# Kernel optimization log

Hardware: AMD Instinct MI355X
Metric: run time of the kernel (lower is better)

## Reference

```python
import jax, jax.numpy as jnp
import numpy as np

B, S, D_IN, D_OUT = 4, 2048, 2048, 2048
EPS = 1e-10


def setup_inputs() -> dict:
    key = jax.random.key(0)
    kx, kw, kb = jax.random.split(key, 3)
    x = jax.random.normal(kx, (B, S, D_IN), dtype=jnp.float32)
    weight = jax.random.normal(kw, (D_OUT, D_IN), dtype=jnp.float32) * 0.02
    bias = jax.random.normal(kb, (D_OUT,), dtype=jnp.float32) * 0.02
    return {"x": x, "weight": weight, "bias": bias}


def reference(x, weight, bias):
    # abs-mean scale over the whole weight matrix (scalar)
    scale = jnp.mean(jnp.abs(weight))
    # ternary quantization: round(w/scale) clamped to {-1, 0, 1}
    w_t = jnp.clip(jnp.round(weight / (scale + EPS)), -1.0, 1.0)
    # straight-through estimator: forward uses w_t*scale, grad flows to weight
    w_ste = weight + jax.lax.stop_gradient(w_t * scale - weight)
    # F.linear: x @ w_ste.T + bias
    return jnp.einsum('bsi,oi->bso', x, w_ste) + bias
```

## Files before the change

kernel.cpp:

```cpp
#include <hip/hip_runtime.h>
#include <hip/hip_bf16.h>
#include <stdint.h>

#define M_DIM 8192
#define N_DIM 2048
#define K_DIM 2048
#define NT    (K_DIM / 64)

typedef float f32x4 __attribute__((ext_vector_type(4)));
typedef short bf16x8 __attribute__((ext_vector_type(8)));

typedef const __attribute__((address_space(1))) char* gp_t;
typedef __attribute__((address_space(3))) char* lp_t;

static __device__ __forceinline__ void gload_lds16(const void* g, void* l) {
  __builtin_amdgcn_global_load_lds((gp_t)(uintptr_t)g, (lp_t)(uint32_t)(uintptr_t)l, 16, 0, 0);
}

static __device__ __forceinline__ unsigned short f2bf(float f) {
  unsigned int u = __float_as_uint(f);
  unsigned int r = (u + 0x7FFFu + ((u >> 16) & 1u)) >> 16;
  return (unsigned short)r;
}

__global__ void absum_partials(const float* __restrict__ w, float* __restrict__ partials) {
  int tid = blockIdx.x * 256 + threadIdx.x;
  const float4* w4 = (const float4*)w;
  float s = 0.f;
#pragma unroll
  for (int i = 0; i < 4; ++i) {
    float4 v = w4[tid + i * 262144];
    s += fabsf(v.x) + fabsf(v.y) + fabsf(v.z) + fabsf(v.w);
  }
#pragma unroll
  for (int off = 32; off > 0; off >>= 1) s += __shfl_down(s, off, 64);
  __shared__ float ls[4];
  if ((threadIdx.x & 63) == 0) ls[threadIdx.x >> 6] = s;
  __syncthreads();
  if (threadIdx.x == 0) partials[blockIdx.x] = (ls[0] + ls[1]) + (ls[2] + ls[3]);
}

__global__ void finalize_scale(const float* __restrict__ partials, float* __restrict__ scale_out) {
  float s = 0.f;
#pragma unroll
  for (int i = 0; i < 4; ++i) s += partials[threadIdx.x + i * 256];
#pragma unroll
  for (int off = 32; off > 0; off >>= 1) s += __shfl_down(s, off, 64);
  __shared__ float ls[4];
  if ((threadIdx.x & 63) == 0) ls[threadIdx.x >> 6] = s;
  __syncthreads();
  if (threadIdx.x == 0)
    scale_out[0] = ((ls[0] + ls[1]) + (ls[2] + ls[3])) * (1.0f / 4194304.0f);
}

__global__ void quant_w(const float* __restrict__ w, const float* __restrict__ scale_p,
                        unsigned short* __restrict__ wt) {
  const float inv = 1.0f / (scale_p[0] + 1e-10f);
  int tid = blockIdx.x * 256 + threadIdx.x;
  float4 v = ((const float4*)w)[tid];
  ushort4 o;
  float t;
  t = fminf(1.f, fmaxf(-1.f, rintf(v.x * inv))); o.x = f2bf(t);
  t = fminf(1.f, fmaxf(-1.f, rintf(v.y * inv))); o.y = f2bf(t);
  t = fminf(1.f, fmaxf(-1.f, rintf(v.z * inv))); o.z = f2bf(t);
  t = fminf(1.f, fmaxf(-1.f, rintf(v.w * inv))); o.w = f2bf(t);
  ((ushort4*)wt)[tid] = o;
}

__global__ void cvt_x(const float* __restrict__ x, unsigned short* __restrict__ xb) {
  int tid = blockIdx.x * 256 + threadIdx.x;
  float4 v = ((const float4*)x)[tid];
  ushort4 o;
  o.x = f2bf(v.x); o.y = f2bf(v.y); o.z = f2bf(v.z); o.w = f2bf(v.w);
  ((ushort4*)xb)[tid] = o;
}


#define VMCNT(n) asm volatile("s_waitcnt vmcnt(" #n ")" ::: "memory")
#define FENCE    asm volatile("" ::: "memory")
#define BARRIER  do { FENCE; __builtin_amdgcn_s_barrier(); FENCE; } while (0)

#define READ_A(mh)                                                                          \
  do {                                                                                      \
    _Pragma("unroll") for (int i = 0; i < 4; ++i) {                                         \
      a_r[i][0] = *(const bf16x8*)(curA + (wr * 128 + (mh) * 64 + i * 16) * 128 + rd_off);  \
      a_r[i][1] = *(const bf16x8*)(curA + (wr * 128 + (mh) * 64 + i * 16) * 128 + 64 + rd_off); \
    }                                                                                       \
  } while (0)

#define READ_B(nh, br)                                                                      \
  do {                                                                                      \
    _Pragma("unroll") for (int j = 0; j < 2; ++j) {                                         \
      br[j][0] = *(const bf16x8*)(curB + (wc * 64 + (nh) * 32 + j * 16) * 128 + rd_off);    \
      br[j][1] = *(const bf16x8*)(curB + (wc * 64 + (nh) * 32 + j * 16) * 128 + 64 + rd_off); \
    }                                                                                       \
  } while (0)

#define MFMA_PH(mh, nh, br)                                                                 \
  do {                                                                                      \
    __builtin_amdgcn_s_setprio(1);                                                          \
    _Pragma("unroll") for (int i = 0; i < 4; ++i)                                           \
      _Pragma("unroll") for (int j = 0; j < 2; ++j)                                         \
        acc[(mh) * 4 + i][(nh) * 2 + j] = __builtin_amdgcn_mfma_f32_16x16x32_bf16(          \
            a_r[i][0], br[j][0], acc[(mh) * 4 + i][(nh) * 2 + j], 0, 0, 0);                 \
    _Pragma("unroll") for (int i = 0; i < 4; ++i)                                           \
      _Pragma("unroll") for (int j = 0; j < 2; ++j)                                         \
        acc[(mh) * 4 + i][(nh) * 2 + j] = __builtin_amdgcn_mfma_f32_16x16x32_bf16(          \
            a_r[i][1], br[j][1], acc[(mh) * 4 + i][(nh) * 2 + j], 0, 0, 0);                 \
    __builtin_amdgcn_s_setprio(0);                                                          \
  } while (0)

#define SA(bufsel, r) gload_lds16(Ag + offA[r] + ktA, ldsb + (bufsel) * 65536 + tid * 16 + (r) * 8192)
#define SB(bufsel, r) gload_lds16(Bg + offB[r] + ktB, ldsb + (bufsel) * 65536 + 32768 + tid * 16 + (r) * 8192)

__global__ void __launch_bounds__(512, 2)
gemm_bt(const unsigned short* __restrict__ A, const unsigned short* __restrict__ Bt,
        const float* __restrict__ bias, const float* __restrict__ scale_p,
        float* __restrict__ out) {
  __shared__ __align__(16) char lds_raw[131072];
  char* ldsb = (char*)lds_raw;

  const int tid = threadIdx.x;
  const int lane = tid & 63;
  const int wid = tid >> 6;
  const int wr = wid >> 2;
  const int wc = wid & 3;
  const int l15 = lane & 15, lhi = lane >> 4;
  const int rd_off = l15 * 128 + ((lhi * 16) ^ (((l15 >> 2) & 1) << 5));

  const int bid = blockIdx.x;
  const int swz = (bid & 7) * 32 + (bid >> 3);
  const int bm = swz >> 3;
  const int bn = swz & 7;
  const int m0 = bm << 8, n0 = bn << 8;

  const int srow = tid >> 3;
  const int scol = ((tid & 7) << 4) ^ (((tid >> 5) & 1) << 5);
  const char* Ag = (const char*)A;
  const char* Bg = (const char*)Bt;
  uint32_t offA[4], offB[4];
#pragma unroll
  for (int r = 0; r < 4; ++r) {
    offA[r] = (uint32_t)(m0 + srow + r * 64) * (K_DIM * 2) + scol;
    offB[r] = (uint32_t)(n0 + srow + r * 64) * (K_DIM * 2) + scol;
  }
  uint32_t ktA = 0, ktB = 0;

  f32x4 acc[8][4];
#pragma unroll
  for (int m = 0; m < 8; ++m)
#pragma unroll
    for (int n = 0; n < 4; ++n) {
      f32x4 z = {0.f, 0.f, 0.f, 0.f};
      acc[m][n] = z;
    }

  SA(0, 0); SA(0, 1); SA(0, 2); SA(0, 3);
  SB(0, 0); SB(0, 1); SB(0, 2); SB(0, 3);
  ktB = 128;
  SB(1, 0); SB(1, 1); SB(1, 2); SB(1, 3);
  ktA = 128; ktB = 256;
  VMCNT(4);
  BARRIER;

  bf16x8 a_r[4][2], b0[2][2], b1[2][2];

  for (int t = 0; t < NT; ++t) {
    const int cb = t & 1;
    const char* curA = ldsb + cb * 65536;
    const char* curB = curA + 32768;

    READ_A(0);
    READ_B(0, b0);
    if (t < NT - 1) { SA(cb ^ 1, 0); SA(cb ^ 1, 1); }
    BARRIER;
    MFMA_PH(0, 0, b0);
    BARRIER;

    READ_B(1, b1);
    if (t < NT - 1) { SA(cb ^ 1, 2); SA(cb ^ 1, 3); ktA += 128; }
    BARRIER;
    MFMA_PH(0, 1, b1);
    BARRIER;

    READ_A(1);
    if (t < NT - 2) { SB(cb, 0); SB(cb, 1); }
    BARRIER;
    MFMA_PH(1, 0, b0);
    BARRIER;

    if (t < NT - 2) {
      SB(cb, 2); SB(cb, 3); ktB += 128;
      VMCNT(4);
    } else {
      VMCNT(0);
    }
    BARRIER;
    MFMA_PH(1, 1, b1);
    BARRIER;
  }

  const float scale = scale_p[0];
#pragma unroll
  for (int n = 0; n < 4; ++n) {
    const int col = n0 + wc * 64 + n * 16 + l15;
    const float bv = bias[col];
#pragma unroll
    for (int m = 0; m < 8; ++m) {
      const int r0 = m0 + wr * 128 + m * 16 + lhi * 4;
      float* op = out + (size_t)r0 * N_DIM + col;
#pragma unroll
      for (int j = 0; j < 4; ++j) op[(size_t)j * N_DIM] = acc[m][n][j] * scale + bv;
    }
  }
}

extern "C" void kernel_launch(void* const* d_in, const int* in_sizes, int n_in,
                              void* d_out, int out_size, void* d_ws, size_t ws_size,
                              hipStream_t stream) {
  (void)in_sizes; (void)n_in; (void)out_size; (void)ws_size;
  const float* x    = (const float*)d_in[0];
  const float* w    = (const float*)d_in[1];
  const float* bias = (const float*)d_in[2];
  float* out = (float*)d_out;

  float* partials = (float*)d_ws;
  float* scale_slot = partials + 1024;
  unsigned short* wt = (unsigned short*)((char*)d_ws + 8192);
  unsigned short* xb = (unsigned short*)((char*)d_ws + 8192 + (size_t)N_DIM * K_DIM * 2);

  absum_partials<<<1024, 256, 0, stream>>>(w, partials);
  finalize_scale<<<1, 256, 0, stream>>>(partials, scale_slot);
  quant_w<<<4096, 256, 0, stream>>>(w, scale_slot, wt);
  cvt_x<<<16384, 256, 0, stream>>>(x, xb);
  gemm_bt<<<256, 512, 0, stream>>>(xb, wt, bias, scale_slot, out);
}
```

Baseline: 100.4 us.

## Fuse preprocessing kernels and switch LDS swizzle to full XOR pattern

Merges the x-to-bf16 conversion and the weight abs-sum partials into one launch, and folds the scale finalization into every quant_w block so each block re-reduces the 1024 partials itself. This cuts the preprocessing from four launches to two, removing launch gaps and the serial single-block finalize step. It also changes the GEMM's LDS store and read swizzle from a single-bit XOR to a 3-bit row XOR to reduce bank conflicts on ds_read. The cost is redundant partial reductions in each quant block.

```diff
diff --git a/kernel.cpp b/kernel.cpp
--- a/kernel.cpp
+++ b/kernel.cpp
@@ -23,39 +23,47 @@
   return (unsigned short)r;
 }
 
-__global__ void absum_partials(const float* __restrict__ w, float* __restrict__ partials) {
-  int tid = blockIdx.x * 256 + threadIdx.x;
-  const float4* w4 = (const float4*)w;
+__global__ void cvt_x_absum(const float* __restrict__ x, unsigned short* __restrict__ xb,
+                            const float* __restrict__ w, float* __restrict__ partials) {
+  const int b = blockIdx.x;
+  if (b < 16384) {
+    int tid = b * 256 + threadIdx.x;
+    float4 v = ((const float4*)x)[tid];
+    ushort4 o;
+    o.x = f2bf(v.x); o.y = f2bf(v.y); o.z = f2bf(v.z); o.w = f2bf(v.w);
+    ((ushort4*)xb)[tid] = o;
+  } else {
+    int tid = (b - 16384) * 256 + threadIdx.x;
+    const float4* w4 = (const float4*)w;
+    float s = 0.f;
+#pragma unroll
+    for (int i = 0; i < 4; ++i) {
+      float4 v = w4[tid + i * 262144];
+      s += fabsf(v.x) + fabsf(v.y) + fabsf(v.z) + fabsf(v.w);
+    }
+#pragma unroll
+    for (int off = 32; off > 0; off >>= 1) s += __shfl_down(s, off, 64);
+    __shared__ float ls[4];
+    if ((threadIdx.x & 63) == 0) ls[threadIdx.x >> 6] = s;
+    __syncthreads();
+    if (threadIdx.x == 0) partials[b - 16384] = (ls[0] + ls[1]) + (ls[2] + ls[3]);
+  }
+}
+
+__global__ void quant_w(const float* __restrict__ w, const float* __restrict__ partials,
+                        unsigned short* __restrict__ wt, float* __restrict__ scale_out) {
+  __shared__ float ls[4];
   float s = 0.f;
 #pragma unroll
-  for (int i = 0; i < 4; ++i) {
-    float4 v = w4[tid + i * 262144];
-    s += fabsf(v.x) + fabsf(v.y) + fabsf(v.z) + fabsf(v.w);
-  }
+  for (int i = 0; i < 4; ++i) s += partials[threadIdx.x + i * 256];
 #pragma unroll
   for (int off = 32; off > 0; off >>= 1) s += __shfl_down(s, off, 64);
-  __shared__ float ls[4];
   if ((threadIdx.x & 63) == 0) ls[threadIdx.x >> 6] = s;
   __syncthreads();
-  if (threadIdx.x == 0) partials[blockIdx.x] = (ls[0] + ls[1]) + (ls[2] + ls[3]);
-}
-
-__global__ void finalize_scale(const float* __restrict__ partials, float* __restrict__ scale_out) {
-  float s = 0.f;
-#pragma unroll
-  for (int i = 0; i < 4; ++i) s += partials[threadIdx.x + i * 256];
-#pragma unroll
-  for (int off = 32; off > 0; off >>= 1) s += __shfl_down(s, off, 64);
-  __shared__ float ls[4];
-  if ((threadIdx.x & 63) == 0) ls[threadIdx.x >> 6] = s;
-  __syncthreads();
-  if (threadIdx.x == 0)
-    scale_out[0] = ((ls[0] + ls[1]) + (ls[2] + ls[3])) * (1.0f / 4194304.0f);
-}
-
-__global__ void quant_w(const float* __restrict__ w, const float* __restrict__ scale_p,
-                        unsigned short* __restrict__ wt) {
-  const float inv = 1.0f / (scale_p[0] + 1e-10f);
+  const float scale = ((ls[0] + ls[1]) + (ls[2] + ls[3])) * (1.0f / 4194304.0f);
+  if (blockIdx.x == 0 && threadIdx.x == 0) scale_out[0] = scale;
+
+  const float inv = 1.0f / (scale + 1e-10f);
   int tid = blockIdx.x * 256 + threadIdx.x;
   float4 v = ((const float4*)w)[tid];
   ushort4 o;
@@ -67,47 +75,39 @@
   ((ushort4*)wt)[tid] = o;
 }
 
-__global__ void cvt_x(const float* __restrict__ x, unsigned short* __restrict__ xb) {
-  int tid = blockIdx.x * 256 + threadIdx.x;
-  float4 v = ((const float4*)x)[tid];
-  ushort4 o;
-  o.x = f2bf(v.x); o.y = f2bf(v.y); o.z = f2bf(v.z); o.w = f2bf(v.w);
-  ((ushort4*)xb)[tid] = o;
-}
-
 
 #define VMCNT(n) asm volatile("s_waitcnt vmcnt(" #n ")" ::: "memory")
 #define FENCE    asm volatile("" ::: "memory")
 #define BARRIER  do { FENCE; __builtin_amdgcn_s_barrier(); FENCE; } while (0)
 
-#define READ_A(mh)                                                                          \
-  do {                                                                                      \
-    _Pragma("unroll") for (int i = 0; i < 4; ++i) {                                         \
-      a_r[i][0] = *(const bf16x8*)(curA + (wr * 128 + (mh) * 64 + i * 16) * 128 + rd_off);  \
-      a_r[i][1] = *(const bf16x8*)(curA + (wr * 128 + (mh) * 64 + i * 16) * 128 + 64 + rd_off); \
-    }                                                                                       \
+#define READ_A(mh)                                                                              \
+  do {                                                                                          \
+    _Pragma("unroll") for (int i = 0; i < 4; ++i) {                                             \
+      a_r[i][0] = *(const bf16x8*)(curA + (wr * 128 + (mh) * 64 + i * 16) * 128 + rd0);         \
+      a_r[i][1] = *(const bf16x8*)(curA + (wr * 128 + (mh) * 64 + i * 16) * 128 + rd1);         \
+    }                                                                                           \
   } while (0)
 
-#define READ_B(nh, br)                                                                      \
-  do {                                                                                      \
-    _Pragma("unroll") for (int j = 0; j < 2; ++j) {                                         \
-      br[j][0] = *(const bf16x8*)(curB + (wc * 64 + (nh) * 32 + j * 16) * 128 + rd_off);    \
-      br[j][1] = *(const bf16x8*)(curB + (wc * 64 + (nh) * 32 + j * 16) * 128 + 64 + rd_off); \
-    }                                                                                       \
+#define READ_B(nh, br)                                                                          \
+  do {                                                                                          \
+    _Pragma("unroll") for (int j = 0; j < 2; ++j) {                                             \
+      br[j][0] = *(const bf16x8*)(curB + (wc * 64 + (nh) * 32 + j * 16) * 128 + rd0);           \
+      br[j][1] = *(const bf16x8*)(curB + (wc * 64 + (nh) * 32 + j * 16) * 128 + rd1);           \
+    }                                                                                           \
   } while (0)
 
-#define MFMA_PH(mh, nh, br)                                                                 \
-  do {                                                                                      \
-    __builtin_amdgcn_s_setprio(1);                                                          \
-    _Pragma("unroll") for (int i = 0; i < 4; ++i)                                           \
-      _Pragma("unroll") for (int j = 0; j < 2; ++j)                                         \
-        acc[(mh) * 4 + i][(nh) * 2 + j] = __builtin_amdgcn_mfma_f32_16x16x32_bf16(          \
-            a_r[i][0], br[j][0], acc[(mh) * 4 + i][(nh) * 2 + j], 0, 0, 0);                 \
-    _Pragma("unroll") for (int i = 0; i < 4; ++i)                                           \
-      _Pragma("unroll") for (int j = 0; j < 2; ++j)                                         \
-        acc[(mh) * 4 + i][(nh) * 2 + j] = __builtin_amdgcn_mfma_f32_16x16x32_bf16(          \
-            a_r[i][1], br[j][1], acc[(mh) * 4 + i][(nh) * 2 + j], 0, 0, 0);                 \
-    __builtin_amdgcn_s_setprio(0);                                                          \
+#define MFMA_PH(mh, nh, br)                                                                     \
+  do {                                                                                          \
+    __builtin_amdgcn_s_setprio(1);                                                              \
+    _Pragma("unroll") for (int i = 0; i < 4; ++i)                                               \
+      _Pragma("unroll") for (int j = 0; j < 2; ++j)                                             \
+        acc[(mh) * 4 + i][(nh) * 2 + j] = __builtin_amdgcn_mfma_f32_16x16x32_bf16(              \
+            a_r[i][0], br[j][0], acc[(mh) * 4 + i][(nh) * 2 + j], 0, 0, 0);                     \
+    _Pragma("unroll") for (int i = 0; i < 4; ++i)                                               \
+      _Pragma("unroll") for (int j = 0; j < 2; ++j)                                             \
+        acc[(mh) * 4 + i][(nh) * 2 + j] = __builtin_amdgcn_mfma_f32_16x16x32_bf16(              \
+            a_r[i][1], br[j][1], acc[(mh) * 4 + i][(nh) * 2 + j], 0, 0, 0);                     \
+    __builtin_amdgcn_s_setprio(0);                                                              \
   } while (0)
 
 #define SA(bufsel, r) gload_lds16(Ag + offA[r] + ktA, ldsb + (bufsel) * 65536 + tid * 16 + (r) * 8192)
@@ -126,7 +126,10 @@
   const int wr = wid >> 2;
   const int wc = wid & 3;
   const int l15 = lane & 15, lhi = lane >> 4;
-  const int rd_off = l15 * 128 + ((lhi * 16) ^ (((l15 >> 2) & 1) << 5));
+
+  const int swzl = (l15 & 7) << 4;
+  const int rd0 = l15 * 128 + ((lhi * 16) ^ swzl);
+  const int rd1 = l15 * 128 + (((lhi * 16) ^ 64) ^ swzl);
 
   const int bid = blockIdx.x;
   const int swz = (bid & 7) * 32 + (bid >> 3);
@@ -135,7 +138,7 @@
   const int m0 = bm << 8, n0 = bn << 8;
 
   const int srow = tid >> 3;
-  const int scol = ((tid & 7) << 4) ^ (((tid >> 5) & 1) << 5);
+  const int scol = (((tid & 7) ^ ((tid >> 3) & 7)) << 4);
   const char* Ag = (const char*)A;
   const char* Bg = (const char*)Bt;
   uint32_t offA[4], offB[4];
@@ -229,9 +232,7 @@
   unsigned short* wt = (unsigned short*)((char*)d_ws + 8192);
   unsigned short* xb = (unsigned short*)((char*)d_ws + 8192 + (size_t)N_DIM * K_DIM * 2);
 
-  absum_partials<<<1024, 256, 0, stream>>>(w, partials);
-  finalize_scale<<<1, 256, 0, stream>>>(partials, scale_slot);
-  quant_w<<<4096, 256, 0, stream>>>(w, scale_slot, wt);
-  cvt_x<<<16384, 256, 0, stream>>>(x, xb);
+  cvt_x_absum<<<17408, 256, 0, stream>>>(x, xb, w, partials);
+  quant_w<<<4096, 256, 0, stream>>>(w, partials, wt, scale_slot);
   gemm_bt<<<256, 512, 0, stream>>>(xb, wt, bias, scale_slot, out);
 }
```

After: 87.02 us. 13.3% less time.
